# Optimization experiments

Hardware: AMD Instinct MI355X
Metric: run time of the kernel (lower is better)

## Reference

```python
import jax, jax.numpy as jnp
import numpy as np

NUM_LAYERS = 2
FEAT = 1024
INP = 2048
OUT = 1024
B, T = 16, 512


def _gru_dir(x_tbf, w_ih, w_hh, b_ih, b_hh):
    # x_tbf: [T, B, in]; torch gate order: r, z, n. Returns [T, B, H].
    H = w_hh.shape[1]
    gx = jnp.einsum('tbi,gi->tbg', x_tbf, w_ih) + b_ih  # [T, B, 3H]

    def step(h, gx_t):
        gh = h @ w_hh.T + b_hh  # [B, 3H]
        xr, xz, xn = jnp.split(gx_t, 3, axis=-1)
        hr, hz, hn = jnp.split(gh, 3, axis=-1)
        r = jax.nn.sigmoid(xr + hr)
        z = jax.nn.sigmoid(xz + hz)
        n = jnp.tanh(xn + r * hn)
        h_new = (1.0 - z) * n + z * h
        return h_new, h_new

    h0 = jnp.zeros((x_tbf.shape[1], H), dtype=x_tbf.dtype)
    _, ys = jax.lax.scan(step, h0, gx)
    return ys


def _bigru_layer(x_tbf, w_ih, w_hh, b_ih, b_hh):
    # w_* stacked over direction: [2, ...]
    fwd = _gru_dir(x_tbf, w_ih[0], w_hh[0], b_ih[0], b_hh[0])
    bwd = jnp.flip(_gru_dir(jnp.flip(x_tbf, axis=0), w_ih[1], w_hh[1], b_ih[1], b_hh[1]), axis=0)
    return jnp.concatenate([fwd, bwd], axis=-1)  # [T, B, 2H]


def setup_inputs() -> dict:
    key = jax.random.key(0)
    ks = jax.random.split(key, 16)
    s = 0.02
    inp = jax.random.normal(ks[0], (B, INP, T), dtype=jnp.float32)
    w_in = jax.random.normal(ks[1], (FEAT, INP), dtype=jnp.float32) * s
    b_in = jnp.zeros((FEAT,), dtype=jnp.float32)
    w_ih_l0 = jax.random.normal(ks[2], (2, 3 * FEAT, FEAT), dtype=jnp.float32) * s
    w_hh_l0 = jax.random.normal(ks[3], (2, 3 * FEAT, FEAT), dtype=jnp.float32) * s
    b_ih_l0 = jax.random.normal(ks[4], (2, 3 * FEAT), dtype=jnp.float32) * s
    b_hh_l0 = jax.random.normal(ks[5], (2, 3 * FEAT), dtype=jnp.float32) * s
    w_ih_l1 = jax.random.normal(ks[6], (2, 3 * FEAT, 2 * FEAT), dtype=jnp.float32) * s
    w_hh_l1 = jax.random.normal(ks[7], (2, 3 * FEAT, FEAT), dtype=jnp.float32) * s
    b_ih_l1 = jax.random.normal(ks[8], (2, 3 * FEAT), dtype=jnp.float32) * s
    b_hh_l1 = jax.random.normal(ks[9], (2, 3 * FEAT), dtype=jnp.float32) * s
    w_out = jax.random.normal(ks[10], (OUT, 2 * FEAT), dtype=jnp.float32) * s
    b_out = jnp.zeros((OUT,), dtype=jnp.float32)
    return dict(inp=inp, w_in=w_in, b_in=b_in,
                w_ih_l0=w_ih_l0, w_hh_l0=w_hh_l0, b_ih_l0=b_ih_l0, b_hh_l0=b_hh_l0,
                w_ih_l1=w_ih_l1, w_hh_l1=w_hh_l1, b_ih_l1=b_ih_l1, b_hh_l1=b_hh_l1,
                w_out=w_out, b_out=b_out)


def reference(inp, w_in, b_in, w_ih_l0, w_hh_l0, b_ih_l0, b_hh_l0,
              w_ih_l1, w_hh_l1, b_ih_l1, b_hh_l1, w_out, b_out):
    # inp: [B, inp_dim, T] -> [B, T, inp_dim]
    x = jnp.transpose(inp, (0, 2, 1))
    x = x @ w_in.T + b_in                      # [B, T, FEAT]
    x = jnp.transpose(x, (1, 0, 2))            # [T, B, FEAT] for scan
    x = _bigru_layer(x, w_ih_l0, w_hh_l0, b_ih_l0, b_hh_l0)  # [T, B, 2F]
    x = _bigru_layer(x, w_ih_l1, w_hh_l1, b_ih_l1, b_hh_l1)  # [T, B, 2F]
    x = jnp.transpose(x, (1, 0, 2))            # [B, T, 2F]
    out = x @ w_out.T + b_out                  # [B, T, OUT]
    return jnp.transpose(out, (0, 2, 1))       # [B, OUT, T]
```

## Files before the change

kernel.cpp:

```cpp
#include <hip/hip_runtime.h>

typedef __attribute__((ext_vector_type(8))) short v8s;
typedef __attribute__((ext_vector_type(4))) float v4f;
typedef __attribute__((ext_vector_type(8))) unsigned short v8u;
typedef __attribute__((ext_vector_type(4))) unsigned short v4u;

__device__ __forceinline__ float bf2f(unsigned short u) {
  unsigned int x = ((unsigned int)u) << 16;
  return __builtin_bit_cast(float, x);
}
__device__ __forceinline__ unsigned short f2bf(float f) {
  unsigned int x = __builtin_bit_cast(unsigned int, f);
  x = x + 0x7FFFu + ((x >> 16) & 1u);
  return (unsigned short)(x >> 16);
}
__device__ __forceinline__ float sigm(float x) { return 1.f / (1.f + __expf(-x)); }
__device__ __forceinline__ float tanh_(float x) {
  x = fminf(fmaxf(x, -15.f), 15.f);
  float e = __expf(2.f * x);
  return (e - 1.f) / (e + 1.f);
}
__device__ __forceinline__ void gll16(const void* g, void* l) {
  __builtin_amdgcn_global_load_lds((const __attribute__((address_space(1))) void*)g,
                                   (__attribute__((address_space(3))) void*)l, 16, 0, 0);
}

__device__ __forceinline__ void st_short_sys(void* p, unsigned int v) {
  asm volatile("global_store_short %0, %1, off sc0 sc1" :: "v"(p), "v"(v) : "memory");
}
__device__ __forceinline__ v8s ld_v8s_sys(const void* p) {
  v8s v;
  asm volatile("global_load_dwordx4 %0, %1, off sc0 sc1" : "=v"(v) : "v"(p) : "memory");
  return v;
}

__global__ void f2bf_kernel(const float* __restrict__ s, unsigned short* __restrict__ d, int n) {
  int i = (blockIdx.x * 256 + threadIdx.x) * 4;
  if (i + 3 < n) {
    v4f v = *(const v4f*)(s + i);
    v4u o;
    #pragma unroll
    for (int j = 0; j < 4; ++j) o[j] = f2bf(v[j]);
    *(v4u*)(d + i) = o;
  }
}

__global__ void transpose_in(const float* __restrict__ inp, unsigned short* __restrict__ X0) {
  int bidx = blockIdx.x;
  int b  = bidx >> 8;
  int i0 = ((bidx >> 3) & 31) << 6;
  int t0 = (bidx & 7) << 6;
  __shared__ float tile[64][65];
  const float* ib = inp + ((size_t)b * 2048 + i0) * 512 + t0;
  #pragma unroll 4
  for (int it = 0; it < 16; ++it) {
    int lin = it * 256 + threadIdx.x;
    int ii = lin >> 6, tt = lin & 63;
    tile[ii][tt] = ib[(size_t)ii * 512 + tt];
  }
  __syncthreads();
  #pragma unroll 4
  for (int it = 0; it < 16; ++it) {
    int lin = it * 256 + threadIdx.x;
    int tt = lin >> 6, ii = lin & 63;
    X0[((size_t)(t0 + tt) * 16 + b) * 2048 + i0 + ii] = f2bf(tile[ii][tt]);
  }
}

template <int SCATTER>
__global__ __launch_bounds__(256, 2) void gemm_bt(
    const unsigned short* __restrict__ A, const unsigned short* __restrict__ W,
    const float* __restrict__ bias, unsigned short* __restrict__ C,
    float* __restrict__ Cf, int M, int N, int K) {
  __shared__ char lds[2][2][16384];

  const int tid = threadIdx.x, lane = tid & 63, wv = tid >> 6;
  const int ntiles = N >> 7;
  const int nwg = gridDim.x;
  const int cpx = nwg >> 3;
  int wgid = blockIdx.x;
  int swz = (wgid & 7) * cpx + (wgid >> 3);
  const int mt = swz / ntiles, nt = swz % ntiles;
  const int wrow = wv >> 1, wcol = wv & 1;

  const unsigned short* Abase = A + (size_t)(mt << 7) * K;
  const unsigned short* Wbase = W + (size_t)(nt << 7) * K;
  const int r8 = lane >> 3, q = lane & 7;
  const int srcoff = (q << 4) ^ (r8 << 4);

  auto stage = [&](int buf, int kt) {
    const char* As = (const char*)(Abase + (size_t)kt * 64);
    const char* Ws = (const char*)(Wbase + (size_t)kt * 64);
    #pragma unroll
    for (int p = 0; p < 4; ++p) {
      int row = (((wv << 2) + p) << 3) + r8;
      int chunk = ((wv << 2) + p) << 10;
      gll16(As + (size_t)row * K * 2 + srcoff, &lds[buf][0][chunk]);
      gll16(Ws + (size_t)row * K * 2 + srcoff, &lds[buf][1][chunk]);
    }
  };

  v4f acc[4][4] = {};
  const int nk = K >> 6;
  stage(0, 0);
  for (int kt = 0; kt < nk; ++kt) {
    __syncthreads();
    if (kt + 1 < nk) stage((kt + 1) & 1, kt + 1);
    const char* la = &lds[kt & 1][0][0] + (((wrow << 6) + (lane & 15)) << 7);
    const char* lb = &lds[kt & 1][1][0] + (((wcol << 6) + (lane & 15)) << 7);
    const int kswz = (lane & 7) << 4;
    #pragma unroll
    for (int kk = 0; kk < 2; ++kk) {
      const int kb = ((kk << 6) + ((lane >> 4) << 4)) ^ kswz;
      v8s af[4], bf[4];
      #pragma unroll
      for (int mi = 0; mi < 4; ++mi) af[mi] = *(const v8s*)(la + (mi << 11) + kb);
      #pragma unroll
      for (int ni = 0; ni < 4; ++ni) bf[ni] = *(const v8s*)(lb + (ni << 11) + kb);
      #pragma unroll
      for (int mi = 0; mi < 4; ++mi)
        #pragma unroll
        for (int ni = 0; ni < 4; ++ni)
          acc[mi][ni] = __builtin_amdgcn_mfma_f32_16x16x32_bf16(af[mi], bf[ni], acc[mi][ni], 0, 0, 0);
    }
  }

  const int gm0 = (mt << 7) + (wrow << 6) + ((lane >> 4) << 2);
  const int gn0 = (nt << 7) + (wcol << 6) + (lane & 15);
  #pragma unroll
  for (int ni = 0; ni < 4; ++ni) {
    const int gn = gn0 + (ni << 4);
    const float bv = bias ? bias[gn] : 0.f;
    #pragma unroll
    for (int mi = 0; mi < 4; ++mi) {
      #pragma unroll
      for (int r = 0; r < 4; ++r) {
        const int gm = gm0 + (mi << 4) + r;
        float v = acc[mi][ni][r] + bv;
        if (SCATTER) {
          Cf[(size_t)(gm & 15) * (1024 * 512) + (size_t)gn * 512 + (gm >> 4)] = v;
        } else {
          C[(size_t)gm * N + gn] = f2bf(v);
        }
      }
    }
  }
}

__global__ __launch_bounds__(256, 1) void gru_recur(
    const unsigned short* __restrict__ gx,
    const float* __restrict__ w_hh,
    const float* __restrict__ b_hh,
    unsigned short* __restrict__ Y,
    int* __restrict__ flags) {
  const int bid = blockIdx.x;
  const int dir = bid & 1;
  const int wg  = bid >> 1;
  const int j0  = wg << 4;
  const int tid = threadIdx.x;
  const int lane = tid & 63, wv = tid >> 6;

  __shared__ unsigned short wsl[3][16][1024];
  __shared__ float red[4][3][16][17];
  __shared__ float bhs[48];

  int* const myflags = flags + dir * 64;

  for (int c = tid; c < 6144; c += 256) {
    int row48 = c >> 7;
    int g = row48 >> 4, jj = row48 & 15;
    int q = c & 127;
    const float* src = w_hh + (((size_t)dir * 3072 + (size_t)g * 1024 + j0 + jj) << 10) + (q << 3);
    v8u v;
    #pragma unroll
    for (int i = 0; i < 8; ++i) v[i] = f2bf(src[i]);
    char* base = (char*)(&wsl[g][jj][0]);
    *(v8u*)(base + ((q << 4) ^ ((jj & 7) << 4))) = v;
  }
  if (tid < 48) bhs[tid] = b_hh[dir * 3072 + (tid >> 4) * 1024 + j0 + (tid & 15)];
  __syncthreads();

  const int b = tid >> 4, jj = tid & 15;
  const size_t ycol = (size_t)dir * 1024;
  const size_t gxc = (size_t)dir * 3072 + j0 + jj;
  float hcur = 0.f;

  int zero = 0;
  asm volatile("" : "+v"(zero));

  for (int s = 0; s < 512; ++s) {
    const int t  = dir ? (511 - s) : s;
    const int tp = dir ? (t + 1) : (t - 1);

    if (s > 0 && wv == 0) {
      int iters = 0;
      for (;;) {
        int v = __hip_atomic_fetch_add(myflags + lane, zero, __ATOMIC_RELAXED,
                                       __HIP_MEMORY_SCOPE_AGENT);
        if (__all(v >= s)) break;
        __builtin_amdgcn_s_sleep(1);
        if (++iters > 3000) break;
      }
    }
    __syncthreads();

    const size_t grow = (size_t)(t * 16 + b);
    float xr = bf2f(gx[grow * 6144 + gxc]);
    float xz = bf2f(gx[grow * 6144 + gxc + 1024]);
    float xn = bf2f(gx[grow * 6144 + gxc + 2048]);

    v4f a0 = {0.f, 0.f, 0.f, 0.f}, a1 = {0.f, 0.f, 0.f, 0.f}, a2 = {0.f, 0.f, 0.f, 0.f};
    if (s > 0) {
      const unsigned short* hrow =
          Y + (size_t)(tp * 16 + (lane & 15)) * 2048 + ycol + (wv << 8) + ((lane >> 4) << 3);
      v8s af[8];
      #pragma unroll
      for (int kk = 0; kk < 8; ++kk) af[kk] = ld_v8s_sys(hrow + (kk << 5));
      asm volatile("s_waitcnt vmcnt(0)" ::: "memory");
      __builtin_amdgcn_sched_barrier(0);
      const char* wb0 = (const char*)(&wsl[0][lane & 15][0]);
      const int swz = (lane & 7) << 4;
      #pragma unroll
      for (int kk = 0; kk < 8; ++kk) {
        const int kb = (((wv << 8) + (kk << 5) + ((lane >> 4) << 3)) << 1) ^ swz;
        v8s b0 = *(const v8s*)(wb0 + kb);
        v8s b1 = *(const v8s*)(wb0 + 32768 + kb);
        v8s b2 = *(const v8s*)(wb0 + 65536 + kb);
        a0 = __builtin_amdgcn_mfma_f32_16x16x32_bf16(af[kk], b0, a0, 0, 0, 0);
        a1 = __builtin_amdgcn_mfma_f32_16x16x32_bf16(af[kk], b1, a1, 0, 0, 0);
        a2 = __builtin_amdgcn_mfma_f32_16x16x32_bf16(af[kk], b2, a2, 0, 0, 0);
      }
    }
    {
      const int rr0 = (lane >> 4) << 2, cc = lane & 15;
      #pragma unroll
      for (int r = 0; r < 4; ++r) {
        red[wv][0][rr0 + r][cc] = a0[r];
        red[wv][1][rr0 + r][cc] = a1[r];
        red[wv][2][rr0 + r][cc] = a2[r];
      }
    }
    __syncthreads();
    float ghr = red[0][0][b][jj] + red[1][0][b][jj] + red[2][0][b][jj] + red[3][0][b][jj] + bhs[jj];
    float ghz = red[0][1][b][jj] + red[1][1][b][jj] + red[2][1][b][jj] + red[3][1][b][jj] + bhs[16 + jj];
    float ghn = red[0][2][b][jj] + red[1][2][b][jj] + red[2][2][b][jj] + red[3][2][b][jj] + bhs[32 + jj];
    float r_ = sigm(xr + ghr);
    float z_ = sigm(xz + ghz);
    float n_ = tanh_(xn + r_ * ghn);
    float h  = (1.f - z_) * n_ + z_ * hcur;
    hcur = h;

    st_short_sys(Y + grow * 2048 + ycol + j0 + jj, (unsigned int)f2bf(h));
    asm volatile("s_waitcnt vmcnt(0)" ::: "memory");
    __syncthreads();
    if (tid == 0 && s < 511)
      __hip_atomic_fetch_add(myflags + wg, 1, __ATOMIC_RELAXED, __HIP_MEMORY_SCOPE_AGENT);
  }
}

extern "C" void kernel_launch(void* const* d_in, const int* in_sizes, int n_in,
                              void* d_out, int out_size, void* d_ws, size_t ws_size,
                              hipStream_t stream) {
  const float* inp     = (const float*)d_in[0];
  const float* w_in    = (const float*)d_in[1];
  const float* b_in    = (const float*)d_in[2];
  const float* w_ih_l0 = (const float*)d_in[3];
  const float* w_hh_l0 = (const float*)d_in[4];
  const float* b_ih_l0 = (const float*)d_in[5];
  const float* b_hh_l0 = (const float*)d_in[6];
  const float* w_ih_l1 = (const float*)d_in[7];
  const float* w_hh_l1 = (const float*)d_in[8];
  const float* b_ih_l1 = (const float*)d_in[9];
  const float* b_hh_l1 = (const float*)d_in[10];
  const float* w_out   = (const float*)d_in[11];
  const float* b_out   = (const float*)d_in[12];

  char* ws = (char*)d_ws;
  size_t off = 0;
  auto carve = [&](size_t bytes) {
    char* p = ws + off;
    off += (bytes + 255) & ~(size_t)255;
    return p;
  };
  unsigned short* GX      = (unsigned short*)carve(8192ull * 6144 * 2);
  unsigned short* X0      = (unsigned short*)carve(8192ull * 2048 * 2);
  unsigned short* XF      = (unsigned short*)carve(8192ull * 1024 * 2);
  unsigned short* Y0      = (unsigned short*)carve(8192ull * 2048 * 2);
  unsigned short* w_in_b  = (unsigned short*)carve(1024ull * 2048 * 2);
  unsigned short* w_l0_b  = (unsigned short*)carve(6144ull * 1024 * 2);
  unsigned short* w_l1_b  = (unsigned short*)carve(6144ull * 2048 * 2);
  unsigned short* w_out_b = (unsigned short*)carve(1024ull * 2048 * 2);
  int* flags              = (int*)carve(4 * 64 * 4);
  unsigned short* Y1 = X0;

  hipMemsetAsync(flags, 0, 4 * 64 * 4, stream);

  f2bf_kernel<<<2097152 / 1024, 256, 0, stream>>>(w_in, w_in_b, 2097152);
  f2bf_kernel<<<6291456 / 1024, 256, 0, stream>>>(w_ih_l0, w_l0_b, 6291456);
  f2bf_kernel<<<12582912 / 1024, 256, 0, stream>>>(w_ih_l1, w_l1_b, 12582912);
  f2bf_kernel<<<2097152 / 1024, 256, 0, stream>>>(w_out, w_out_b, 2097152);

  transpose_in<<<4096, 256, 0, stream>>>(inp, X0);

  gemm_bt<0><<<512, 256, 0, stream>>>(X0, w_in_b, b_in, XF, nullptr, 8192, 1024, 2048);
  gemm_bt<0><<<3072, 256, 0, stream>>>(XF, w_l0_b, b_ih_l0, GX, nullptr, 8192, 6144, 1024);
  gru_recur<<<128, 256, 0, stream>>>(GX, w_hh_l0, b_hh_l0, Y0, flags);
  gemm_bt<0><<<3072, 256, 0, stream>>>(Y0, w_l1_b, b_ih_l1, GX, nullptr, 8192, 6144, 2048);
  gru_recur<<<128, 256, 0, stream>>>(GX, w_hh_l1, b_hh_l1, Y1, flags + 128);
  gemm_bt<1><<<512, 256, 0, stream>>>(Y1, w_out_b, b_out, nullptr, (float*)d_out, 8192, 1024, 2048);
}
```

Measured before the change: 5.862 ms.

## Poll flags per-wave with plain loads, store flag values, prefetch next gx

The inter-workgroup step barrier changes in three ways. Every wave now polls its own flag slice with system-coherent plain loads instead of wave 0 doing atomic fetch-adds, which removes one __syncthreads per step. Producers write s+1 with a plain store instead of an atomic increment. The next step's input-gate values are loaded before the h store and wait, so their latency is hidden behind the barrier. The trade-offs are more polling traffic from all waves and a lower spin timeout, which means correctness depends on store visibility ordering.

New measurement: 5.096 ms. 13.1% less time.

```diff
diff --git a/kernel.cpp b/kernel.cpp
--- a/kernel.cpp
+++ b/kernel.cpp
@@ -27,6 +27,15 @@
 
 __device__ __forceinline__ void st_short_sys(void* p, unsigned int v) {
   asm volatile("global_store_short %0, %1, off sc0 sc1" :: "v"(p), "v"(v) : "memory");
+}
+__device__ __forceinline__ void st_int_sys(void* p, int v) {
+  asm volatile("global_store_dword %0, %1, off sc0 sc1" :: "v"(p), "v"(v) : "memory");
+}
+__device__ __forceinline__ int ld_int_sys(const void* p) {
+  int v;
+  asm volatile("global_load_dword %0, %1, off sc0 sc1" : "=v"(v) : "v"(p) : "memory");
+  asm volatile("s_waitcnt vmcnt(0)" ::: "memory");
+  return v;
 }
 __device__ __forceinline__ v8s ld_v8s_sys(const void* p) {
   v8s v;
@@ -185,29 +194,30 @@
   const size_t gxc = (size_t)dir * 3072 + j0 + jj;
   float hcur = 0.f;
 
-  int zero = 0;
-  asm volatile("" : "+v"(zero));
+  const int* const fp = myflags + ((wv << 4) + (lane & 15));
+
+  float xr, xz, xn;
+  {
+    const int t0i = dir ? 511 : 0;
+    const size_t g0 = (size_t)(t0i * 16 + b) * 6144 + gxc;
+    xr = bf2f(gx[g0]);
+    xz = bf2f(gx[g0 + 1024]);
+    xn = bf2f(gx[g0 + 2048]);
+  }
 
   for (int s = 0; s < 512; ++s) {
     const int t  = dir ? (511 - s) : s;
     const int tp = dir ? (t + 1) : (t - 1);
 
-    if (s > 0 && wv == 0) {
+    if (s > 0) {
       int iters = 0;
       for (;;) {
-        int v = __hip_atomic_fetch_add(myflags + lane, zero, __ATOMIC_RELAXED,
-                                       __HIP_MEMORY_SCOPE_AGENT);
+        int v = ld_int_sys(fp);
         if (__all(v >= s)) break;
         __builtin_amdgcn_s_sleep(1);
-        if (++iters > 3000) break;
+        if (++iters > 2000) break;
       }
     }
-    __syncthreads();
-
-    const size_t grow = (size_t)(t * 16 + b);
-    float xr = bf2f(gx[grow * 6144 + gxc]);
-    float xz = bf2f(gx[grow * 6144 + gxc + 1024]);
-    float xn = bf2f(gx[grow * 6144 + gxc + 2048]);
 
     v4f a0 = {0.f, 0.f, 0.f, 0.f}, a1 = {0.f, 0.f, 0.f, 0.f}, a2 = {0.f, 0.f, 0.f, 0.f};
     if (s > 0) {
@@ -250,11 +260,22 @@
     float h  = (1.f - z_) * n_ + z_ * hcur;
     hcur = h;
 
-    st_short_sys(Y + grow * 2048 + ycol + j0 + jj, (unsigned int)f2bf(h));
+    float nxr = 0.f, nxz = 0.f, nxn = 0.f;
+    if (s < 511) {
+      const int tn = dir ? (510 - s) : (s + 1);
+      const size_t gn = (size_t)(tn * 16 + b) * 6144 + gxc;
+      nxr = bf2f(gx[gn]);
+      nxz = bf2f(gx[gn + 1024]);
+      nxn = bf2f(gx[gn + 2048]);
+    }
+
+    st_short_sys(Y + (size_t)(t * 16 + b) * 2048 + ycol + j0 + jj, (unsigned int)f2bf(h));
     asm volatile("s_waitcnt vmcnt(0)" ::: "memory");
     __syncthreads();
     if (tid == 0 && s < 511)
-      __hip_atomic_fetch_add(myflags + wg, 1, __ATOMIC_RELAXED, __HIP_MEMORY_SCOPE_AGENT);
+      st_int_sys(myflags + wg, s + 1);
+
+    xr = nxr; xz = nxz; xn = nxn;
   }
 }
 
```
